# Kernel tuning notes

Hardware: AMD Instinct MI355X
Metric: run time of the kernel (lower is better)

Reference implementation:

```python
import jax, jax.numpy as jnp
import numpy as np

L, D, V = 8, 1024, 32000
DT_MIN, DT_MAX = 0.01, 0.1
EPS = 1e-5


def _layer_norm(x, w, b):
    mu = jnp.mean(x, -1, keepdims=True)
    var = jnp.var(x, -1, keepdims=True)
    return (x - mu) * jax.lax.rsqrt(var + EPS) * w + b


def _encode(ids):
    # deterministic phase encoding of tokens onto the unit phase sphere
    theta = 2.0 * jnp.pi * ids.astype(jnp.float32) / V  # [B,S]
    k = jnp.arange(1, D // 2 + 1, dtype=jnp.float32)
    ang = theta[..., None] * k  # [B,S,D/2]
    return jnp.concatenate([jnp.cos(ang), jnp.sin(ang)], -1) / jnp.sqrt(jnp.float32(D))


def _flux(s, mask):
    # attention-like causal score from state self-interaction
    score = jnp.einsum('bqd,bkd->bqk', s, s) / jnp.sqrt(jnp.float32(D))
    score = jnp.where(mask, score, 0.0)
    return jnp.einsum('bqk,bkd->bqd', score, s), score


def _evolve_with_tunneling(s, dt, mask):
    # Heun-Euler (predictor-corrector) integration step
    k1, score = _flux(s, mask)
    mid = s + dt * k1
    k2, _ = _flux(mid, mask)
    ev = s + 0.5 * dt * (k1 + k2)
    # quantum tunneling: boost low-energy states proportionally to dt/dt_max
    energy = jnp.linalg.norm(ev, axis=-1)  # [B,S]
    thr = jnp.mean(energy, axis=-1, keepdims=True)
    tunnel = energy < thr
    strength = dt / DT_MAX  # [B,1,1]
    ev = jnp.where(tunnel[..., None], ev * (1.0 + strength), ev)
    ratio = jnp.mean(tunnel.astype(jnp.float32))
    return ev, score, ratio


def setup_inputs() -> dict:
    key = jax.random.key(0)
    ks = jax.random.split(key, 4)
    B, S = 2, 2048
    input_ids = jax.random.randint(ks[0], (B, S), 0, V)
    labels = jax.random.randint(ks[1], (B, S), 0, V)
    proj_w = jax.random.normal(ks[2], (L, D, D), jnp.float32) * 0.02
    proj_b = jnp.zeros((L, D), jnp.float32)
    ln_w = jnp.ones((L, D), jnp.float32)
    ln_b = jnp.zeros((L, D), jnp.float32)
    fln_w = jnp.ones((D,), jnp.float32)
    fln_b = jnp.zeros((D,), jnp.float32)
    out_w = jax.random.normal(ks[3], (D, V), jnp.float32) * 0.02
    return dict(input_ids=input_ids, labels=labels, proj_w=proj_w, proj_b=proj_b,
                ln_w=ln_w, ln_b=ln_b, fln_w=fln_w, fln_b=fln_b, out_w=out_w)


def reference(input_ids, labels, proj_w, proj_b, ln_w, ln_b, fln_w, fln_b, out_w):
    B, S = input_ids.shape
    mask = jnp.tril(jnp.ones((S, S), dtype=bool))
    # deterministic timestep (midpoint of [dt_min, dt_max]); dropout in eval mode
    dt = jnp.full((B, 1, 1), 0.5 * (DT_MIN + DT_MAX), jnp.float32)
    states = _encode(input_ids)
    for i in range(L):
        ev, _score, _ratio = _evolve_with_tunneling(states, dt, mask)
        states = _layer_norm(ev @ proj_w[i] + proj_b[i], ln_w[i], ln_b[i])
    states = _layer_norm(states, fln_w, fln_b)
    # normalized quantum projection to vocab
    energy = jnp.linalg.norm(states, axis=-1, keepdims=True)
    logits = (states / (energy + 1e-12)) @ out_w  # [B,S,V]
    # shifted cross-entropy
    sl = logits[:, :-1, :].reshape(-1, V)
    tl = labels[:, 1:].reshape(-1)
    logp = jax.nn.log_softmax(sl, axis=-1)
    loss = -jnp.mean(jnp.take_along_axis(logp, tl[:, None], axis=1))
    return logits, loss
```

## Files before the change

### kernel.cpp

```cpp
#include <hip/hip_runtime.h>

#define LL 8
#define DD 1024
#define VV 32000
#define SS 2048
#define BB 2
#define NROWS 4096
#define DT_STEP 0.055f
#define HALF_DT 0.0275f
#define TUNNEL_SCALE 1.55f

typedef __attribute__((ext_vector_type(8))) short bf16x8;
typedef __attribute__((ext_vector_type(4))) float f32x4;

static __device__ __forceinline__ float bf2f(unsigned short u){
  union { unsigned int i; float f; } v; v.i = ((unsigned int)u) << 16; return v.f;
}
static __device__ __forceinline__ unsigned short f2bf(float f){
  union { float f; unsigned int i; } v; v.f = f;
  unsigned int r = v.i + 0x7fffu + ((v.i >> 16) & 1u);
  return (unsigned short)(r >> 16);
}

static __device__ __forceinline__ void gl16(const unsigned short* g, unsigned short* l){
  __builtin_amdgcn_global_load_lds(
      (const __attribute__((address_space(1))) unsigned int*)g,
      (__attribute__((address_space(3))) unsigned int*)l, 16, 0, 0);
}

__device__ __forceinline__ float block_sum256(float v, volatile float* scratch){
  #pragma unroll
  for (int off = 32; off; off >>= 1) v += __shfl_down(v, off, 64);
  int w = threadIdx.x >> 6, lane = threadIdx.x & 63;
  __syncthreads();
  if (lane == 0) scratch[w] = v;
  __syncthreads();
  return scratch[0] + scratch[1] + scratch[2] + scratch[3];
}

__global__ void encode_kernel(const int* __restrict__ ids, float* __restrict__ s_f32,
                              unsigned short* __restrict__ hi, unsigned short* __restrict__ lo){
  int row = blockIdx.x;
  int t = threadIdx.x;
  float theta = 6.28318530717958647692f * (float)ids[row] / 32000.0f;
  #pragma unroll
  for (int i = 0; i < 2; ++i){
    int kk = t + i * 256;
    float ang = theta * (float)(kk + 1);
    float sv, cv; sincosf(ang, &sv, &cv);
    float c = cv * 0.03125f, s = sv * 0.03125f;
    long b0 = (long)row * DD + kk, b1 = b0 + 512;
    s_f32[b0] = c; s_f32[b1] = s;
    unsigned short ch = f2bf(c); hi[b0] = ch; lo[b0] = f2bf(c - bf2f(ch));
    unsigned short sh = f2bf(s); hi[b1] = sh; lo[b1] = f2bf(s - bf2f(sh));
  }
}

__global__ void transpose_bf16_pair_kernel(const unsigned short* __restrict__ in_hi,
                                           const unsigned short* __restrict__ in_lo,
                                           unsigned short* __restrict__ out_hi,
                                           unsigned short* __restrict__ out_lo,
                                           int R, int C){
  __shared__ __align__(16) unsigned short tile[64][80];
  int zz = blockIdx.z;
  const unsigned short* in = (zz & 1) ? in_lo : in_hi;
  unsigned short* out = (zz & 1) ? out_lo : out_hi;
  long ib = (long)(zz >> 1) * R * C;
  int c0 = blockIdx.x * 64, r0 = blockIdx.y * 64;
  int t = threadIdx.x;
  #pragma unroll
  for (int i = 0; i < 2; ++i){
    int j = t + i * 256; int row = j >> 3, cc = j & 7;
    *(uint4*)&tile[row][cc * 8] = *(const uint4*)(in + ib + (long)(r0 + row) * C + c0 + cc * 8);
  }
  __syncthreads();
  #pragma unroll
  for (int i = 0; i < 2; ++i){
    int j = t + i * 256; int orow = j >> 3, cc = j & 7;
    union { unsigned short u[8]; uint4 v; } tmp;
    #pragma unroll
    for (int e = 0; e < 8; ++e) tmp.u[e] = tile[cc * 8 + e][orow];
    *(uint4*)(out + ib + (long)(c0 + orow) * R + r0 + cc * 8) = tmp.v;
  }
}

template<bool SPLIT>
__global__ void transpose_f32_bf16_kernel(const float* __restrict__ in,
                                          unsigned short* __restrict__ ohi,
                                          unsigned short* __restrict__ olo, int R, int C){
  __shared__ float tile[64][68];
  long ib = (long)blockIdx.z * R * C;
  int c0 = blockIdx.x * 64, r0 = blockIdx.y * 64;
  int t = threadIdx.x;
  #pragma unroll
  for (int i = 0; i < 4; ++i){
    int j = t + i * 256; int row = j >> 4, cc = j & 15;
    *(float4*)&tile[row][cc * 4] = *(const float4*)(in + ib + (long)(r0 + row) * C + c0 + cc * 4);
  }
  __syncthreads();
  #pragma unroll
  for (int i = 0; i < 2; ++i){
    int j = t + i * 256; int orow = j >> 3, cc = j & 7;
    union { unsigned short u[8]; uint4 v; } th, tl;
    #pragma unroll
    for (int e = 0; e < 8; ++e){
      float v = tile[cc * 8 + e][orow];
      unsigned short h = f2bf(v); th.u[e] = h;
      if (SPLIT) tl.u[e] = f2bf(v - bf2f(h));
    }
    long ob = ib + (long)(c0 + orow) * R + r0 + cc * 8;
    *(uint4*)(ohi + ob) = th.v;
    if (SPLIT) *(uint4*)(olo + ob) = tl.v;
  }
}

template<int OUTMODE, int CAUSAL>
__global__ __launch_bounds__(512, 4)
void gemm_nt_kernel(const unsigned short* __restrict__ Ahi, const unsigned short* __restrict__ Alo,
                    const unsigned short* __restrict__ Bhi, const unsigned short* __restrict__ Blo,
                    float* __restrict__ C, unsigned short* __restrict__ Chi,
                    unsigned short* __restrict__ Clo, const float* __restrict__ bias,
                    const float* __restrict__ Sf, const float* __restrict__ K1f,
                    int K, int lda, int ldb, int ldc, int MT, int NT,
                    long batchA, long batchB, long batchC, float alpha)
{
  const int bz = blockIdx.y;
  const int nwg = MT * NT;
  const int q = nwg >> 3, r = nwg & 7;
  const int xcd = blockIdx.x & 7, off = blockIdx.x >> 3;
  const int wg = (xcd < r ? xcd * (q + 1) : r * (q + 1) + (xcd - r) * q) + off;
  const int band = wg / (NT << 3), rem = wg - band * (NT << 3);
  const int mt = (band << 3) + (rem & 7), nt = rem >> 3;
  if (CAUSAL == 1 && nt > mt) return;
  const int m0 = mt << 7, n0 = nt << 7;
  int Keff = K;
  if (CAUSAL == 2){ int kl = (mt + 1) << 7; Keff = kl < K ? kl : K; }

  __shared__ __align__(16) unsigned short sA[2][128][64];
  __shared__ __align__(16) unsigned short sB[2][128][64];

  const int tid = threadIdx.x;
  const int lane = tid & 63;
  const int w = tid >> 6;
  const int wr = w >> 2, wc = w & 3;
  const int fr = lane & 15, fc = lane >> 4;
  const int fr7 = fr & 7;

  f32x4 acc[4][2];
  #pragma unroll
  for (int i = 0; i < 4; ++i)
    #pragma unroll
    for (int j = 0; j < 2; ++j) acc[i][j] = (f32x4){0.f, 0.f, 0.f, 0.f};

  const int srow = tid >> 3, slot = tid & 7;
  const int cont = slot ^ (srow & 7);
  const long aoff = (long)bz * batchA, boff = (long)bz * batchB;
  const int gcol = (cont & 3) << 3;
  const unsigned short* gA = (cont >= 4 ? Alo : Ahi) + aoff + (long)(m0 + srow) * lda + gcol;
  const unsigned short* gB = (cont >= 4 ? Blo : Bhi) + boff + (long)(n0 + srow) * ldb + gcol;
  const long rstepA = 64L * lda, rstepB = 64L * ldb;
  const int wofs = w << 9;

  const int oh = (fc ^ fr7) << 4;
  const int ol = ((4 + fc) ^ fr7) << 4;

  const int ntiles = Keff >> 5;

  gl16(gA,          &sA[0][0][0] + wofs);
  gl16(gA + rstepA, &sA[0][0][0] + 4096 + wofs);
  gl16(gB,          &sB[0][0][0] + wofs);
  gl16(gB + rstepB, &sB[0][0][0] + 4096 + wofs);

  int cur = 0;
  for (int t = 0; t < ntiles; ++t){
    const bool stg = (t < ntiles - 1);
    const long nk = (long)(t + 1) << 5;
    const char* bA_ = (const char*)&sA[cur][0][0];
    const char* bB_ = (const char*)&sB[cur][0][0];
    bf16x8 ah_[4], al_[4];

    if (stg){
      gl16(gA + nk,          &sA[cur ^ 1][0][0] + wofs);
      gl16(gA + nk + rstepA, &sA[cur ^ 1][0][0] + 4096 + wofs);
      asm volatile("s_waitcnt vmcnt(2)" ::: "memory");
    } else {
      asm volatile("s_waitcnt vmcnt(0)" ::: "memory");
    }
    asm volatile("s_barrier" ::: "memory");
    #pragma unroll
    for (int mi = 0; mi < 4; ++mi){
      const char* p_ = bA_ + (wr * 64 + mi * 16 + fr) * 128;
      ah_[mi] = *(const bf16x8*)(p_ + oh);
      al_[mi] = *(const bf16x8*)(p_ + ol);
    }
    {
      const char* pb_ = bB_ + (wc * 32 + fr) * 128;
      bf16x8 bh_ = *(const bf16x8*)(pb_ + oh);
      bf16x8 bl_ = *(const bf16x8*)(pb_ + ol);
      __builtin_amdgcn_s_setprio(1);
      #pragma unroll
      for (int mi = 0; mi < 4; ++mi){
        acc[mi][0] = __builtin_amdgcn_mfma_f32_16x16x32_bf16(ah_[mi], bh_, acc[mi][0], 0, 0, 0);
        acc[mi][0] = __builtin_amdgcn_mfma_f32_16x16x32_bf16(ah_[mi], bl_, acc[mi][0], 0, 0, 0);
        acc[mi][0] = __builtin_amdgcn_mfma_f32_16x16x32_bf16(al_[mi], bh_, acc[mi][0], 0, 0, 0);
      }
      __builtin_amdgcn_s_setprio(0);
    }

    if (stg){
      gl16(gB + nk,          &sB[cur ^ 1][0][0] + wofs);
      gl16(gB + nk + rstepB, &sB[cur ^ 1][0][0] + 4096 + wofs);
    }
    asm volatile("s_barrier" ::: "memory");
    {
      const char* pb_ = bB_ + (wc * 32 + 16 + fr) * 128;
      bf16x8 bh_ = *(const bf16x8*)(pb_ + oh);
      bf16x8 bl_ = *(const bf16x8*)(pb_ + ol);
      __builtin_amdgcn_s_setprio(1);
      #pragma unroll
      for (int mi = 0; mi < 4; ++mi){
        acc[mi][1] = __builtin_amdgcn_mfma_f32_16x16x32_bf16(ah_[mi], bh_, acc[mi][1], 0, 0, 0);
        acc[mi][1] = __builtin_amdgcn_mfma_f32_16x16x32_bf16(ah_[mi], bl_, acc[mi][1], 0, 0, 0);
        acc[mi][1] = __builtin_amdgcn_mfma_f32_16x16x32_bf16(al_[mi], bh_, acc[mi][1], 0, 0, 0);
      }
      __builtin_amdgcn_s_setprio(0);
    }
    cur ^= 1;
  }

  const long coff = (long)bz * batchC;
  const int rb0 = m0 + wr * 64 + fc * 4;
  const int cb0 = n0 + wc * 32 + fr;
  #pragma unroll
  for (int mi = 0; mi < 4; ++mi){
    #pragma unroll
    for (int ni = 0; ni < 2; ++ni){
      #pragma unroll
      for (int rg = 0; rg < 4; ++rg){
        int row = rb0 + mi * 16 + rg;
        int col = cb0 + ni * 16;
        float v = acc[mi][ni][rg] * alpha;
        long idx = coff + (long)row * ldc + col;
        if (OUTMODE == 0){
          if (bias) v += bias[col];
          C[idx] = v;
        } else if (OUTMODE == 2){
          if (CAUSAL == 1 && col > row) v = 0.0f;
          unsigned short h = f2bf(v);
          Chi[idx] = h;
          Clo[idx] = f2bf(v - bf2f(h));
        } else if (OUTMODE == 3){
          C[idx] = v;
          float m = Sf[idx] + DT_STEP * v;
          unsigned short h = f2bf(m);
          Chi[idx] = h;
          Clo[idx] = f2bf(m - bf2f(h));
        } else {
          C[idx] = Sf[idx] + HALF_DT * (K1f[idx] + v);
        }
      }
    }
  }
}

__global__ __launch_bounds__(512, 2)
void gemm256_kernel(const unsigned short* __restrict__ A,
                    const unsigned short* __restrict__ Bt,
                    float* __restrict__ C,
                    float* __restrict__ psum)
{
  const int MT = 16, NT = 125;
  const int nwg = MT * NT;
  const int q = nwg >> 3, r = nwg & 7;
  const int xcd = blockIdx.x & 7, off = blockIdx.x >> 3;
  const int wg = (xcd < r ? xcd * (q + 1) : r * (q + 1) + (xcd - r) * q) + off;
  const int band = wg / (NT << 3), rem = wg - band * (NT << 3);
  const int mt = (band << 3) + (rem & 7), nt = rem >> 3;
  const int m0 = mt << 8, n0 = nt << 8;

  __shared__ __align__(16) unsigned short sA[2][256][64];
  __shared__ __align__(16) unsigned short sB[2][256][64];

  const int tid = threadIdx.x;
  const int lane = tid & 63;
  const int w = tid >> 6;
  const int wr = w >> 2, wc = w & 3;
  const int fr = lane & 15, fc = lane >> 4;
  const int fr7 = fr & 7;

  f32x4 acc[8][4];
  #pragma unroll
  for (int i = 0; i < 8; ++i)
    #pragma unroll
    for (int j = 0; j < 4; ++j) acc[i][j] = (f32x4){0.f, 0.f, 0.f, 0.f};

  const int srow = tid >> 3, slot = tid & 7;
  const int cont = slot ^ (srow & 7);
  const unsigned short* gA = A  + (long)(m0 + srow) * DD + (cont << 3);
  const unsigned short* gB = Bt + (long)(n0 + srow) * DD + (cont << 3);
  const int wofs = w << 9;

  #define SGA(buf, kt, i) gl16(gA + (long)((i) * 64) * DD + (kt), &sA[buf][0][0] + (i) * 4096 + wofs)
  #define SGB(buf, kt, i) gl16(gB + (long)((i) * 64) * DD + (kt), &sB[buf][0][0] + (i) * 4096 + wofs)

  const int oh = (fc ^ fr7) << 4;
  const int ol = ((4 + fc) ^ fr7) << 4;

  #pragma unroll
  for (int i = 0; i < 4; ++i){ SGA(0, 0, i); SGB(0, 0, i); }

  int cur = 0;
  for (int t = 0; t < 16; ++t){
    const int nk = (t + 1) << 6;
    const bool stg = (t < 15);
    const char* bA = (const char*)&sA[cur][0][0];
    const char* bB = (const char*)&sB[cur][0][0];
    bf16x8 aq[4][2], bq[4][2];

    if (stg){ SGA(cur ^ 1, nk, 0); SGA(cur ^ 1, nk, 1);
              asm volatile("s_waitcnt vmcnt(2)" ::: "memory"); }
    else    { asm volatile("s_waitcnt vmcnt(0)" ::: "memory"); }
    asm volatile("s_barrier" ::: "memory");
    #pragma unroll
    for (int mi = 0; mi < 4; ++mi){
      const char* p = bA + (wr * 128 + mi * 16 + fr) * 128;
      aq[mi][0] = *(const bf16x8*)(p + oh);
      aq[mi][1] = *(const bf16x8*)(p + ol);
    }
    #pragma unroll
    for (int ni = 0; ni < 2; ++ni){
      const char* p = bB + (wc * 64 + ni * 16 + fr) * 128;
      bq[ni][0] = *(const bf16x8*)(p + oh);
      bq[ni][1] = *(const bf16x8*)(p + ol);
    }
    __builtin_amdgcn_s_setprio(1);
    #pragma unroll
    for (int ks = 0; ks < 2; ++ks)
      #pragma unroll
      for (int mi = 0; mi < 4; ++mi)
        #pragma unroll
        for (int ni = 0; ni < 2; ++ni)
          acc[mi][ni] = __builtin_amdgcn_mfma_f32_16x16x32_bf16(aq[mi][ks], bq[ni][ks], acc[mi][ni], 0, 0, 0);
    __builtin_amdgcn_s_setprio(0);

    if (stg){ SGA(cur ^ 1, nk, 2); SGA(cur ^ 1, nk, 3); }
    asm volatile("s_barrier" ::: "memory");
    #pragma unroll
    for (int ni = 2; ni < 4; ++ni){
      const char* p = bB + (wc * 64 + ni * 16 + fr) * 128;
      bq[ni][0] = *(const bf16x8*)(p + oh);
      bq[ni][1] = *(const bf16x8*)(p + ol);
    }
    __builtin_amdgcn_s_setprio(1);
    #pragma unroll
    for (int ks = 0; ks < 2; ++ks)
      #pragma unroll
      for (int mi = 0; mi < 4; ++mi)
        #pragma unroll
        for (int ni = 2; ni < 4; ++ni)
          acc[mi][ni] = __builtin_amdgcn_mfma_f32_16x16x32_bf16(aq[mi][ks], bq[ni][ks], acc[mi][ni], 0, 0, 0);
    __builtin_amdgcn_s_setprio(0);

    if (stg){ SGB(cur ^ 1, nk, 0); SGB(cur ^ 1, nk, 1); }
    asm volatile("s_barrier" ::: "memory");
    #pragma unroll
    for (int mi = 0; mi < 4; ++mi){
      const char* p = bA + (wr * 128 + (mi + 4) * 16 + fr) * 128;
      aq[mi][0] = *(const bf16x8*)(p + oh);
      aq[mi][1] = *(const bf16x8*)(p + ol);
    }
    __builtin_amdgcn_s_setprio(1);
    #pragma unroll
    for (int ks = 0; ks < 2; ++ks)
      #pragma unroll
      for (int mi = 0; mi < 4; ++mi)
        #pragma unroll
        for (int ni = 2; ni < 4; ++ni)
          acc[mi + 4][ni] = __builtin_amdgcn_mfma_f32_16x16x32_bf16(aq[mi][ks], bq[ni][ks], acc[mi + 4][ni], 0, 0, 0);
    __builtin_amdgcn_s_setprio(0);

    if (stg){ SGB(cur ^ 1, nk, 2); SGB(cur ^ 1, nk, 3); }
    asm volatile("s_barrier" ::: "memory");
    __builtin_amdgcn_s_setprio(1);
    #pragma unroll
    for (int ks = 0; ks < 2; ++ks)
      #pragma unroll
      for (int mi = 0; mi < 4; ++mi)
        #pragma unroll
        for (int ni = 0; ni < 2; ++ni)
          acc[mi + 4][ni] = __builtin_amdgcn_mfma_f32_16x16x32_bf16(aq[mi][ks], bq[ni][ks], acc[mi + 4][ni], 0, 0, 0);
    __builtin_amdgcn_s_setprio(0);

    cur ^= 1;
  }
  #undef SGA
  #undef SGB

  const int rb0 = m0 + wr * 128 + fc * 4;
  const int cb0 = n0 + wc * 64 + fr;
  #pragma unroll
  for (int mi = 0; mi < 8; ++mi){
    #pragma unroll
    for (int ni = 0; ni < 4; ++ni){
      #pragma unroll
      for (int rg = 0; rg < 4; ++rg){
        C[(long)(rb0 + mi * 16 + rg) * VV + cb0 + ni * 16] = acc[mi][ni][rg];
      }
    }
  }

  #pragma unroll
  for (int mi = 0; mi < 8; ++mi){
    #pragma unroll
    for (int rg = 0; rg < 4; ++rg){
      float s4 = __expf(acc[mi][0][rg]) + __expf(acc[mi][1][rg])
               + __expf(acc[mi][2][rg]) + __expf(acc[mi][3][rg]);
      #pragma unroll
      for (int o = 1; o < 16; o <<= 1) s4 += __shfl_xor(s4, o, 64);
      if (fr == 0){
        long pidx = ((long)(rb0 + mi * 16 + rg) << 9) + nt * 4 + wc;
        psum[pidx] = s4;
      }
    }
  }
}

__global__ void energy_kernel(const float* __restrict__ ev, float* __restrict__ energy){
  int row = blockIdx.x, t = threadIdx.x;
  long base = (long)row * DD + t * 4;
  float4 v = *(const float4*)(ev + base);
  __shared__ float scratch[4];
  float n2 = block_sum256(v.x*v.x + v.y*v.y + v.z*v.z + v.w*v.w, scratch);
  if (t == 0) energy[row] = sqrtf(n2);
}

__global__ void mean_energy_kernel(const float* __restrict__ energy, float* __restrict__ thr){
  int b = blockIdx.x, t = threadIdx.x;
  float s = 0.f;
  for (int j = t; j < SS; j += 256) s += energy[b * SS + j];
  __shared__ float scratch[4];
  float tot = block_sum256(s, scratch);
  if (t == 0) thr[b] = tot * (1.0f / SS);
}

__global__ void tunnel_kernel(const float* __restrict__ ev, const float* __restrict__ energy,
                              const float* __restrict__ thr,
                              unsigned short* __restrict__ hi, unsigned short* __restrict__ lo){
  int row = blockIdx.x, t = threadIdx.x;
  float scale = (energy[row] < thr[row >> 11]) ? TUNNEL_SCALE : 1.0f;
  long base = (long)row * DD + t * 4;
  float4 v = *(const float4*)(ev + base);
  v.x *= scale; v.y *= scale; v.z *= scale; v.w *= scale;
  ushort4 hv, lv;
  hv.x = f2bf(v.x); lv.x = f2bf(v.x - bf2f(hv.x));
  hv.y = f2bf(v.y); lv.y = f2bf(v.y - bf2f(hv.y));
  hv.z = f2bf(v.z); lv.z = f2bf(v.z - bf2f(hv.z));
  hv.w = f2bf(v.w); lv.w = f2bf(v.w - bf2f(hv.w));
  *(ushort4*)(hi + base) = hv; *(ushort4*)(lo + base) = lv;
}

__global__ void ln_kernel(const float* __restrict__ h, const float* __restrict__ w,
                          const float* __restrict__ b, float* __restrict__ s_f32,
                          unsigned short* __restrict__ hi, unsigned short* __restrict__ lo){
  int row = blockIdx.x, t = threadIdx.x;
  long base = (long)row * DD + t * 4;
  float4 xv = *(const float4*)(h + base);
  __shared__ float scratch[4];
  float sum = block_sum256(xv.x + xv.y + xv.z + xv.w, scratch);
  float ssq = block_sum256(xv.x*xv.x + xv.y*xv.y + xv.z*xv.z + xv.w*xv.w, scratch);
  float mu = sum * (1.0f / DD);
  float var = ssq * (1.0f / DD) - mu * mu;
  float rstd = rsqrtf(var + 1e-5f);
  float4 wv = *(const float4*)(w + t * 4), bv = *(const float4*)(b + t * 4);
  float y0 = (xv.x - mu) * rstd * wv.x + bv.x;
  float y1 = (xv.y - mu) * rstd * wv.y + bv.y;
  float y2 = (xv.z - mu) * rstd * wv.z + bv.z;
  float y3 = (xv.w - mu) * rstd * wv.w + bv.w;
  float4 o; o.x = y0; o.y = y1; o.z = y2; o.w = y3;
  *(float4*)(s_f32 + base) = o;
  ushort4 hv, lv;
  hv.x = f2bf(y0); lv.x = f2bf(y0 - bf2f(hv.x));
  hv.y = f2bf(y1); lv.y = f2bf(y1 - bf2f(hv.y));
  hv.z = f2bf(y2); lv.z = f2bf(y2 - bf2f(hv.z));
  hv.w = f2bf(y3); lv.w = f2bf(y3 - bf2f(hv.w));
  *(ushort4*)(hi + base) = hv; *(ushort4*)(lo + base) = lv;
}

__global__ void fln_kernel(const float* __restrict__ s, const float* __restrict__ w,
                           const float* __restrict__ b, unsigned short* __restrict__ uhi){
  int row = blockIdx.x, t = threadIdx.x;
  long base = (long)row * DD + t * 4;
  float4 xv = *(const float4*)(s + base);
  __shared__ float scratch[4];
  float sum = block_sum256(xv.x + xv.y + xv.z + xv.w, scratch);
  float ssq = block_sum256(xv.x*xv.x + xv.y*xv.y + xv.z*xv.z + xv.w*xv.w, scratch);
  float mu = sum * (1.0f / DD);
  float var = ssq * (1.0f / DD) - mu * mu;
  float rstd = rsqrtf(var + 1e-5f);
  float4 wv = *(const float4*)(w + t * 4), bv = *(const float4*)(b + t * 4);
  float y0 = (xv.x - mu) * rstd * wv.x + bv.x;
  float y1 = (xv.y - mu) * rstd * wv.y + bv.y;
  float y2 = (xv.z - mu) * rstd * wv.z + bv.z;
  float y3 = (xv.w - mu) * rstd * wv.w + bv.w;
  float n2 = block_sum256(y0*y0 + y1*y1 + y2*y2 + y3*y3, scratch);
  float inv = 1.0f / (sqrtf(n2) + 1e-12f);
  ushort4 o;
  o.x = f2bf(y0 * inv); o.y = f2bf(y1 * inv);
  o.z = f2bf(y2 * inv); o.w = f2bf(y3 * inv);
  *(ushort4*)(uhi + base) = o;
}

__global__ void lse_reduce_kernel(const float* __restrict__ psum,
                                  const float* __restrict__ logits, const int* __restrict__ labels,
                                  float* __restrict__ lrow){
  int idx = blockIdx.x;
  int b = idx / (SS - 1), qq = idx - b * (SS - 1);
  int row = b * SS + qq;
  int t = threadIdx.x;
  float l = 0.f;
  for (int p = t; p < 500; p += 64) l += psum[((long)row << 9) + p];
  #pragma unroll
  for (int o = 1; o < 64; o <<= 1) l += __shfl_xor(l, o, 64);
  if (t == 0){
    float lse = __logf(l);
    float tl = logits[(long)row * VV + labels[row + 1]];
    lrow[idx] = lse - tl;
  }
}

__global__ void loss_reduce_kernel(const float* __restrict__ lrow, float* __restrict__ dst){
  __shared__ float scratch[4];
  float s = 0.f;
  for (int j = threadIdx.x; j < BB * (SS - 1); j += 256) s += lrow[j];
  float tot = block_sum256(s, scratch);
  if (threadIdx.x == 0) dst[0] = tot / (float)(BB * (SS - 1));
}

extern "C" void kernel_launch(void* const* d_in, const int* in_sizes, int n_in,
                              void* d_out, int out_size, void* d_ws, size_t ws_size,
                              hipStream_t stream) {
  const int*   ids    = (const int*)d_in[0];
  const int*   labels = (const int*)d_in[1];
  const float* proj_w = (const float*)d_in[2];
  const float* proj_b = (const float*)d_in[3];
  const float* ln_w   = (const float*)d_in[4];
  const float* ln_b   = (const float*)d_in[5];
  const float* fln_w  = (const float*)d_in[6];
  const float* fln_b  = (const float*)d_in[7];
  const float* out_w  = (const float*)d_in[8];
  float* out = (float*)d_out;

  char* ws = (char*)d_ws;
  float*          s_f32 = (float*)(ws + 0);
  unsigned short* op_hi = (unsigned short*)(ws + 16777216);
  unsigned short* op_lo = (unsigned short*)(ws + 25165824);
  unsigned short* T_hi  = (unsigned short*)(ws + 33554432);
  unsigned short* T_lo  = (unsigned short*)(ws + 41943040);
  float*          k1    = (float*)(ws + 50331648);
  float*          k2    = (float*)(ws + 67108864);
  unsigned short* sc_hi = (unsigned short*)(ws + 83886080);
  unsigned short* sc_lo = (unsigned short*)(ws + 92274688);
  unsigned short* WhiT  = (unsigned short*)(ws + 100663296);
  unsigned short* WloT  = (unsigned short*)(ws + 117440512);
  float*          energy= (float*)(ws + 134217728);
  float*          thr   = (float*)(ws + 134234112);
  float*          lrow  = (float*)(ws + 134234368);
  unsigned short* owT   = T_hi;
  float*          psum  = (float*)(ws + 0);

  transpose_f32_bf16_kernel<true><<<dim3(16, 16, 8), 256, 0, stream>>>(proj_w, WhiT, WloT, DD, DD);
  encode_kernel<<<NROWS, 256, 0, stream>>>(ids, s_f32, op_hi, op_lo);
  transpose_bf16_pair_kernel<<<dim3(16, 32, 4), 256, 0, stream>>>(op_hi, op_lo, T_hi, T_lo, SS, DD);

  for (int l = 0; l < LL; ++l){
    gemm_nt_kernel<2, 1><<<dim3(256, 2), 512, 0, stream>>>(
        op_hi, op_lo, op_hi, op_lo, nullptr, sc_hi, sc_lo, nullptr, nullptr, nullptr,
        DD, DD, DD, SS, 16, 16, (long)SS * DD, (long)SS * DD, (long)SS * SS, 0.03125f);
    gemm_nt_kernel<3, 2><<<dim3(128, 2), 512, 0, stream>>>(
        sc_hi, sc_lo, T_hi, T_lo, k1, op_hi, op_lo, nullptr, s_f32, nullptr,
        SS, SS, SS, DD, 16, 8, (long)SS * SS, (long)DD * SS, (long)SS * DD, 1.0f);
    transpose_bf16_pair_kernel<<<dim3(16, 32, 4), 256, 0, stream>>>(op_hi, op_lo, T_hi, T_lo, SS, DD);
    gemm_nt_kernel<2, 1><<<dim3(256, 2), 512, 0, stream>>>(
        op_hi, op_lo, op_hi, op_lo, nullptr, sc_hi, sc_lo, nullptr, nullptr, nullptr,
        DD, DD, DD, SS, 16, 16, (long)SS * DD, (long)SS * DD, (long)SS * SS, 0.03125f);
    gemm_nt_kernel<4, 2><<<dim3(128, 2), 512, 0, stream>>>(
        sc_hi, sc_lo, T_hi, T_lo, k2, nullptr, nullptr, nullptr, s_f32, k1,
        SS, SS, SS, DD, 16, 8, (long)SS * SS, (long)DD * SS, (long)SS * DD, 1.0f);
    energy_kernel<<<NROWS, 256, 0, stream>>>(k2, energy);
    mean_energy_kernel<<<BB, 256, 0, stream>>>(energy, thr);
    tunnel_kernel<<<NROWS, 256, 0, stream>>>(k2, energy, thr, op_hi, op_lo);
    gemm_nt_kernel<0, 0><<<dim3(256, 1), 512, 0, stream>>>(
        op_hi, op_lo, WhiT + (long)l * DD * DD, WloT + (long)l * DD * DD,
        k1, nullptr, nullptr, proj_b + l * DD, nullptr, nullptr,
        DD, DD, DD, DD, 32, 8, 0, 0, 0, 1.0f);
    ln_kernel<<<NROWS, 256, 0, stream>>>(k1, ln_w + l * DD, ln_b + l * DD, s_f32, op_hi, op_lo);
    if (l < LL - 1){
      transpose_bf16_pair_kernel<<<dim3(16, 32, 4), 256, 0, stream>>>(op_hi, op_lo, T_hi, T_lo, SS, DD);
    }
  }

  transpose_f32_bf16_kernel<false><<<dim3(500, 16, 1), 256, 0, stream>>>(out_w, owT, nullptr, DD, VV);
  fln_kernel<<<NROWS, 256, 0, stream>>>(s_f32, fln_w, fln_b, op_hi);
  gemm256_kernel<<<2000, 512, 0, stream>>>(op_hi, owT, out, psum);
  lse_reduce_kernel<<<BB * (SS - 1), 64, 0, stream>>>(psum, out, labels, lrow);
  loss_reduce_kernel<<<1, 256, 0, stream>>>(lrow, out + (long)NROWS * VV);
}
```

Before: 2.826 ms.

## Split-K causal score@state GEMMs to balance work and fuse mid-state transpose

```diff
diff --git a/kernel.cpp b/kernel.cpp
--- a/kernel.cpp
+++ b/kernel.cpp
@@ -120,21 +120,33 @@
                     const unsigned short* __restrict__ Bhi, const unsigned short* __restrict__ Blo,
                     float* __restrict__ C, unsigned short* __restrict__ Chi,
                     unsigned short* __restrict__ Clo, const float* __restrict__ bias,
-                    const float* __restrict__ Sf, const float* __restrict__ K1f,
                     int K, int lda, int ldb, int ldc, int MT, int NT,
                     long batchA, long batchB, long batchC, float alpha)
 {
   const int bz = blockIdx.y;
-  const int nwg = MT * NT;
-  const int q = nwg >> 3, r = nwg & 7;
-  const int xcd = blockIdx.x & 7, off = blockIdx.x >> 3;
-  const int wg = (xcd < r ? xcd * (q + 1) : r * (q + 1) + (xcd - r) * q) + off;
-  const int band = wg / (NT << 3), rem = wg - band * (NT << 3);
-  const int mt = (band << 3) + (rem & 7), nt = rem >> 3;
+  int mt, nt, ks = 0;
+  {
+    const int nwg = MT * NT;
+    const int q = nwg >> 3, r = nwg & 7;
+    const int xcd = blockIdx.x & 7, off = blockIdx.x >> 3;
+    const int wg = (xcd < r ? xcd * (q + 1) : r * (q + 1) + (xcd - r) * q) + off;
+    if (CAUSAL == 3){
+      if (wg < 128){ ks = 0; mt = wg >> 3; nt = wg & 7; }
+      else { int w2 = wg - 128; ks = 1; mt = 8 + (w2 >> 3); nt = w2 & 7; }
+    } else {
+      const int band = wg / (NT << 3), rem = wg - band * (NT << 3);
+      mt = (band << 3) + (rem & 7); nt = rem >> 3;
+    }
+  }
   if (CAUSAL == 1 && nt > mt) return;
   const int m0 = mt << 7, n0 = nt << 7;
-  int Keff = K;
-  if (CAUSAL == 2){ int kl = (mt + 1) << 7; Keff = kl < K ? kl : K; }
+  int kstart = 0, kend = K;
+  if (CAUSAL == 2){ int kl = (mt + 1) << 7; kend = kl < K ? kl : K; }
+  if (CAUSAL == 3){
+    kstart = ks << 10;
+    int kl = (mt + 1) << 7, kc = kstart + 1024;
+    kend = kl < kc ? kl : kc;
+  }
 
   __shared__ __align__(16) unsigned short sA[2][128][64];
   __shared__ __align__(16) unsigned short sB[2][128][64];
@@ -164,17 +176,17 @@
   const int oh = (fc ^ fr7) << 4;
   const int ol = ((4 + fc) ^ fr7) << 4;
 
-  const int ntiles = Keff >> 5;
-
-  gl16(gA,          &sA[0][0][0] + wofs);
-  gl16(gA + rstepA, &sA[0][0][0] + 4096 + wofs);
-  gl16(gB,          &sB[0][0][0] + wofs);
-  gl16(gB + rstepB, &sB[0][0][0] + 4096 + wofs);
+  const int ntiles = (kend - kstart) >> 5;
+
+  gl16(gA + kstart,          &sA[0][0][0] + wofs);
+  gl16(gA + kstart + rstepA, &sA[0][0][0] + 4096 + wofs);
+  gl16(gB + kstart,          &sB[0][0][0] + wofs);
+  gl16(gB + kstart + rstepB, &sB[0][0][0] + 4096 + wofs);
 
   int cur = 0;
   for (int t = 0; t < ntiles; ++t){
     const bool stg = (t < ntiles - 1);
-    const long nk = (long)(t + 1) << 5;
+    const long nk = kstart + ((long)(t + 1) << 5);
     const char* bA_ = (const char*)&sA[cur][0][0];
     const char* bB_ = (const char*)&sB[cur][0][0];
     bf16x8 ah_[4], al_[4];
@@ -229,6 +241,7 @@
   }
 
   const long coff = (long)bz * batchC;
+  float* Cout = (OUTMODE == 5 && ks) ? (float*)Chi : C;
   const int rb0 = m0 + wr * 64 + fc * 4;
   const int cb0 = n0 + wc * 32 + fr;
   #pragma unroll
@@ -249,14 +262,8 @@
           unsigned short h = f2bf(v);
           Chi[idx] = h;
           Clo[idx] = f2bf(v - bf2f(h));
-        } else if (OUTMODE == 3){
-          C[idx] = v;
-          float m = Sf[idx] + DT_STEP * v;
-          unsigned short h = f2bf(m);
-          Chi[idx] = h;
-          Clo[idx] = f2bf(m - bf2f(h));
         } else {
-          C[idx] = Sf[idx] + HALF_DT * (K1f[idx] + v);
+          Cout[idx] = v;
         }
       }
     }
@@ -425,12 +432,74 @@
   }
 }
 
-__global__ void energy_kernel(const float* __restrict__ ev, float* __restrict__ energy){
+__global__ void mid_trans_kernel(const float* __restrict__ s, float* __restrict__ k1,
+                                 const float* __restrict__ k1b,
+                                 unsigned short* __restrict__ ohi, unsigned short* __restrict__ olo,
+                                 unsigned short* __restrict__ thi, unsigned short* __restrict__ tlo){
+  __shared__ float tile[64][68];
+  int c0 = blockIdx.x * 64, r0g = blockIdx.y * 64;
+  int t = threadIdx.x;
+  #pragma unroll
+  for (int i = 0; i < 4; ++i){
+    int j = t + i * 256; int row = j >> 4, cc = (j & 15) * 4;
+    long idx = (long)(r0g + row) * DD + c0 + cc;
+    float4 a = *(const float4*)(k1 + idx);
+    if (((r0g + row) & 2047) >= 1024){
+      float4 b = *(const float4*)(k1b + idx);
+      a.x += b.x; a.y += b.y; a.z += b.z; a.w += b.w;
+    }
+    *(float4*)(k1 + idx) = a;
+    float4 sv = *(const float4*)(s + idx);
+    float4 m;
+    m.x = sv.x + DT_STEP * a.x; m.y = sv.y + DT_STEP * a.y;
+    m.z = sv.z + DT_STEP * a.z; m.w = sv.w + DT_STEP * a.w;
+    *(float4*)&tile[row][cc] = m;
+    ushort4 hv, lv;
+    hv.x = f2bf(m.x); lv.x = f2bf(m.x - bf2f(hv.x));
+    hv.y = f2bf(m.y); lv.y = f2bf(m.y - bf2f(hv.y));
+    hv.z = f2bf(m.z); lv.z = f2bf(m.z - bf2f(hv.z));
+    hv.w = f2bf(m.w); lv.w = f2bf(m.w - bf2f(hv.w));
+    *(ushort4*)(ohi + idx) = hv; *(ushort4*)(olo + idx) = lv;
+  }
+  __syncthreads();
+  long tb = (long)(r0g >> 11) * DD * SS;
+  int sb = r0g & 2047;
+  #pragma unroll
+  for (int i = 0; i < 2; ++i){
+    int j = t + i * 256; int ocol = j >> 3, cc = (j & 7) * 8;
+    union { unsigned short u[8]; uint4 v; } th, tl;
+    #pragma unroll
+    for (int e = 0; e < 8; ++e){
+      float v = tile[cc + e][ocol];
+      unsigned short h = f2bf(v);
+      th.u[e] = h; tl.u[e] = f2bf(v - bf2f(h));
+    }
+    long ob = tb + (long)(c0 + ocol) * SS + sb + cc;
+    *(uint4*)(thi + ob) = th.v;
+    *(uint4*)(tlo + ob) = tl.v;
+  }
+}
+
+__global__ void ev_energy_kernel(const float* __restrict__ s, const float* __restrict__ k1,
+                                 float* __restrict__ k2, const float* __restrict__ k2b,
+                                 float* __restrict__ energy){
   int row = blockIdx.x, t = threadIdx.x;
   long base = (long)row * DD + t * 4;
-  float4 v = *(const float4*)(ev + base);
+  float4 sv = *(const float4*)(s + base);
+  float4 av = *(const float4*)(k1 + base);
+  float4 bv = *(const float4*)(k2 + base);
+  if ((row & 2047) >= 1024){
+    float4 cv = *(const float4*)(k2b + base);
+    bv.x += cv.x; bv.y += cv.y; bv.z += cv.z; bv.w += cv.w;
+  }
+  float4 ev;
+  ev.x = sv.x + HALF_DT * (av.x + bv.x);
+  ev.y = sv.y + HALF_DT * (av.y + bv.y);
+  ev.z = sv.z + HALF_DT * (av.z + bv.z);
+  ev.w = sv.w + HALF_DT * (av.w + bv.w);
+  *(float4*)(k2 + base) = ev;
   __shared__ float scratch[4];
-  float n2 = block_sum256(v.x*v.x + v.y*v.y + v.z*v.z + v.w*v.w, scratch);
+  float n2 = block_sum256(ev.x*ev.x + ev.y*ev.y + ev.z*ev.z + ev.w*ev.w, scratch);
   if (t == 0) energy[row] = sqrtf(n2);
 }
 
@@ -567,6 +636,8 @@
   float*          lrow  = (float*)(ws + 134234368);
   unsigned short* owT   = T_hi;
   float*          psum  = (float*)(ws + 0);
+  float*          k1b   = k2;
+  float*          k2b   = (float*)(ws + 16777216);
 
   transpose_f32_bf16_kernel<true><<<dim3(16, 16, 8), 256, 0, stream>>>(proj_w, WhiT, WloT, DD, DD);
   encode_kernel<<<NROWS, 256, 0, stream>>>(ids, s_f32, op_hi, op_lo);
@@ -574,24 +645,24 @@
 
   for (int l = 0; l < LL; ++l){
     gemm_nt_kernel<2, 1><<<dim3(256, 2), 512, 0, stream>>>(
-        op_hi, op_lo, op_hi, op_lo, nullptr, sc_hi, sc_lo, nullptr, nullptr, nullptr,
+        op_hi, op_lo, op_hi, op_lo, nullptr, sc_hi, sc_lo, nullptr,
         DD, DD, DD, SS, 16, 16, (long)SS * DD, (long)SS * DD, (long)SS * SS, 0.03125f);
-    gemm_nt_kernel<3, 2><<<dim3(128, 2), 512, 0, stream>>>(
-        sc_hi, sc_lo, T_hi, T_lo, k1, op_hi, op_lo, nullptr, s_f32, nullptr,
-        SS, SS, SS, DD, 16, 8, (long)SS * SS, (long)DD * SS, (long)SS * DD, 1.0f);
-    transpose_bf16_pair_kernel<<<dim3(16, 32, 4), 256, 0, stream>>>(op_hi, op_lo, T_hi, T_lo, SS, DD);
+    gemm_nt_kernel<5, 3><<<dim3(192, 2), 512, 0, stream>>>(
+        sc_hi, sc_lo, T_hi, T_lo, k1, (unsigned short*)k1b, nullptr, nullptr,
+        SS, SS, SS, DD, 24, 8, (long)SS * SS, (long)DD * SS, (long)SS * DD, 1.0f);
+    mid_trans_kernel<<<dim3(16, 64), 256, 0, stream>>>(s_f32, k1, k1b, op_hi, op_lo, T_hi, T_lo);
     gemm_nt_kernel<2, 1><<<dim3(256, 2), 512, 0, stream>>>(
-        op_hi, op_lo, op_hi, op_lo, nullptr, sc_hi, sc_lo, nullptr, nullptr, nullptr,
+        op_hi, op_lo, op_hi, op_lo, nullptr, sc_hi, sc_lo, nullptr,
         DD, DD, DD, SS, 16, 16, (long)SS * DD, (long)SS * DD, (long)SS * SS, 0.03125f);
-    gemm_nt_kernel<4, 2><<<dim3(128, 2), 512, 0, stream>>>(
-        sc_hi, sc_lo, T_hi, T_lo, k2, nullptr, nullptr, nullptr, s_f32, k1,
-        SS, SS, SS, DD, 16, 8, (long)SS * SS, (long)DD * SS, (long)SS * DD, 1.0f);
-    energy_kernel<<<NROWS, 256, 0, stream>>>(k2, energy);
+    gemm_nt_kernel<5, 3><<<dim3(192, 2), 512, 0, stream>>>(
+        sc_hi, sc_lo, T_hi, T_lo, k2, (unsigned short*)k2b, nullptr, nullptr,
+        SS, SS, SS, DD, 24, 8, (long)SS * SS, (long)DD * SS, (long)SS * DD, 1.0f);
+    ev_energy_kernel<<<NROWS, 256, 0, stream>>>(s_f32, k1, k2, k2b, energy);
     mean_energy_kernel<<<BB, 256, 0, stream>>>(energy, thr);
     tunnel_kernel<<<NROWS, 256, 0, stream>>>(k2, energy, thr, op_hi, op_lo);
     gemm_nt_kernel<0, 0><<<dim3(256, 1), 512, 0, stream>>>(
         op_hi, op_lo, WhiT + (long)l * DD * DD, WloT + (long)l * DD * DD,
-        k1, nullptr, nullptr, proj_b + l * DD, nullptr, nullptr,
+        k1, nullptr, nullptr, proj_b + l * DD,
         DD, DD, DD, DD, 32, 8, 0, 0, 0, 1.0f);
     ln_kernel<<<NROWS, 256, 0, stream>>>(k1, ln_w + l * DD, ln_b + l * DD, s_f32, op_hi, op_lo);
     if (l < LL - 1){
```

Measured after the change: 2.624 ms. 7.1% less time.
